# Kernel optimization log

Hardware: AMD Instinct MI355X
Metric: run time of the kernel (lower is better)

## Reference

```python
import jax, jax.numpy as jnp
import numpy as np

N, E, G = 10000, 100000, 64
NB, EMB, S, COUT, LMAX = 16, 16, 8, 16, 2
RMAX = 4.0
WNUM = (LMAX + 1) * COUT * S * S  # 3072 per-edge TP weights


def setup_inputs() -> dict:
    key = jax.random.key(0)
    ks = jax.random.split(key, 16)
    def lin(k, i, o):
        return (jax.random.normal(k, (i, o), jnp.float32) / np.sqrt(i)).astype(jnp.float32)
    return {
        "pos": jax.random.normal(ks[0], (N, 3), jnp.float32),
        "A": jax.random.randint(ks[1], (N,), 0, 10),
        "batch": jnp.sort(jax.random.randint(ks[2], (N,), 0, G)),
        "edge_src": jax.random.randint(ks[3], (E,), 0, N),
        "edge_dst": jax.random.randint(ks[4], (E,), 0, N),
        "edge_shifts": jnp.zeros((E, 3), jnp.float32),
        "cell": jax.random.normal(ks[5], (G, 3, 3), jnp.float32),
        "emb_table": jax.random.normal(ks[6], (10, EMB), jnp.float32),
        "mlp_w1": lin(ks[7], EMB, 64), "mlp_b1": jnp.zeros((64,), jnp.float32),
        "mlp_w2": lin(ks[8], 64, S), "mlp_b2": jnp.zeros((S,), jnp.float32),
        "fc_w1": lin(ks[9], NB, 64), "fc_b1": jnp.zeros((64,), jnp.float32),
        "fc_w2": lin(ks[10], 64, 64), "fc_b2": jnp.zeros((64,), jnp.float32),
        "fc_w3": lin(ks[11], 64, WNUM), "fc_b3": jnp.zeros((WNUM,), jnp.float32),
    }


def _forward(pos, edge_shifts, cell, emb_table, mlp_w1, mlp_b1, mlp_w2, mlp_b2,
             fc_w1, fc_b1, fc_w2, fc_b2, fc_w3, fc_b3, A, batch, edge_src, edge_dst):
    # periodic-image edge vectors: shifts @ cell[graph of src node]
    shift = jnp.einsum('ei,eij->ej', edge_shifts, cell[batch[edge_src]])
    vec = pos[edge_dst] - pos[edge_src] + shift                     # (E,3)
    r = jnp.linalg.norm(vec, axis=1)                                # (E,)
    n = vec / jnp.maximum(r, 1e-9)[:, None]                         # unit edge direction
    # per-node scalar features: atom_mlp(atom_embedding(A))
    Ai = jax.nn.silu(emb_table[A] @ mlp_w1 + mlp_b1) @ mlp_w2 + mlp_b2  # (N,S)
    # radial basis: gaussian soft-one-hot on [0, RMAX] with cutoff, * sqrt(NB)
    vals = jnp.linspace(0.0, RMAX, NB + 2)[1:-1]
    step = RMAX / (NB + 1)
    emb = jnp.exp(-(((r[:, None] - vals) / step) ** 2)) / 1.12 * np.sqrt(NB)  # (E,NB)
    # radial MLP -> per-edge tensor-product weights
    h = jax.nn.silu(emb @ fc_w1 + fc_b1)
    h = jax.nn.silu(h @ fc_w2 + fc_b2)
    W = (h @ fc_w3 + fc_b3).reshape(E, LMAX + 1, COUT, S, S)        # (E,L,Cout,C1,C2)
    # f_in rank-L block is Ai[src] x n^{(x)L}; x2 is scalar Ai[dst].
    # The Cartesian TP factorizes: channel mixing once, then attach n^{(x)L}.
    fs, fd = Ai[edge_src], Ai[edge_dst]                             # (E,S)
    m = jnp.einsum('eloab,ea,eb->elo', W, fs, fd)                   # (E,L,Cout)
    out0 = m[:, 0]                                                  # (E,Cout)       rank 0
    out1 = m[:, 1, :, None] * n[:, None, :]                         # (E,Cout,3)     rank 1
    n2 = n[:, :, None] * n[:, None, :]                              # (E,3,3)
    out2 = m[:, 2, :, None, None] * n2[:, None]                     # (E,Cout,3,3)   rank 2
    ef = jnp.concatenate([out0, out1.reshape(E, -1), out2.reshape(E, -1)], axis=-1)  # (E, 13*Cout)
    # scatter-sum to destination nodes, normalize by neighbor count (clamped to 1)
    cnt = jnp.maximum(jax.ops.segment_sum(jnp.ones((E,), ef.dtype), edge_dst, num_segments=N), 1.0)
    return jax.ops.segment_sum(ef, edge_dst, num_segments=N) / cnt[:, None]  # (N, 208)


def reference(pos, A, batch, edge_src, edge_dst, edge_shifts, cell, emb_table,
              mlp_w1, mlp_b1, mlp_w2, mlp_b2, fc_w1, fc_b1, fc_w2, fc_b2, fc_w3, fc_b3):
    return _forward(pos, edge_shifts, cell, emb_table, mlp_w1, mlp_b1, mlp_w2, mlp_b2,
                    fc_w1, fc_b1, fc_w2, fc_b2, fc_w3, fc_b3, A, batch, edge_src, edge_dst)
```

## Files before the change

kernel.cpp:

```cpp
#include <hip/hip_runtime.h>
#include <math.h>
#include <stdint.h>


typedef float  f32x4  __attribute__((ext_vector_type(4)));
typedef short  s16x8  __attribute__((ext_vector_type(8)));
typedef __bf16 bf16x8 __attribute__((ext_vector_type(8)));

__device__ __forceinline__ float silu_f(float x) {
    return x / (1.0f + __expf(-x));
}

__device__ __forceinline__ void split8(f32x4 a, f32x4 b, s16x8& hi, s16x8& lo) {
    bf16x8 h8, l8;
    #pragma unroll
    for (int i = 0; i < 4; ++i) {
        float z = a[i]; __bf16 zh = (__bf16)z; h8[i] = zh; l8[i] = (__bf16)(z - (float)zh);
        float y = b[i]; __bf16 yh = (__bf16)y; h8[4 + i] = yh; l8[4 + i] = (__bf16)(y - (float)yh);
    }
    hi = __builtin_bit_cast(s16x8, h8);
    lo = __builtin_bit_cast(s16x8, l8);
}

__global__ __launch_bounds__(256) void k_setup(const float* __restrict__ w3,
                                               const float* __restrict__ b3,
                                               ushort* __restrict__ wz,
                                               const int* __restrict__ A,
                                               const float* __restrict__ embt,
                                               const float* __restrict__ w1,
                                               const float* __restrict__ b1,
                                               const float* __restrict__ w2,
                                               const float* __restrict__ b2,
                                               float* __restrict__ Ai,
                                               const int* __restrict__ edst,
                                               int* __restrict__ deg,
                                               int N, int E, int aiB) {
    const int b = blockIdx.x;
    const int tid = threadIdx.x;
    if (b < 780) {
        int t = b * 256 + tid;
        int j    = t & 7;
        int l    = (t >> 3) & 63;
        int rest = t >> 9;
        int tt   = rest % 3;
        int s    = rest / 3;
        int lo   = tt * 16 + (l & 15);
        int kl   = (l >> 4) * 8 + j;
        float v;
        if (s < 128) {
            int ab = s >> 1;
            int c  = (s & 1) * 32 + kl;
            v = w3[c * 3072 + lo * 64 + ab];
        } else {
            int ab = (s - 128) * 32 + kl;
            v = b3[lo * 64 + ab];
        }
        __bf16 hi  = (__bf16)v;
        __bf16 lor = (__bf16)(v - (float)hi);
        size_t base = (size_t)(s * 3 + tt) * 2 * 512 + l * 8 + j;
        wz[base]       = __builtin_bit_cast(ushort, hi);
        wz[base + 512] = __builtin_bit_cast(ushort, lor);
    } else if (b < 780 + aiB) {
        int i = (b - 780) * 256 + tid;
        if (i >= N) return;
        float e[16];
        const float* er = embt + A[i] * 16;
        #pragma unroll
        for (int k = 0; k < 16; ++k) e[k] = er[k];
        float h1[64];
        #pragma unroll
        for (int j = 0; j < 64; ++j) {
            float a = b1[j];
            #pragma unroll
            for (int k = 0; k < 16; ++k) a = fmaf(e[k], w1[k * 64 + j], a);
            h1[j] = silu_f(a);
        }
        #pragma unroll
        for (int o = 0; o < 8; ++o) {
            float a = b2[o];
            #pragma unroll
            for (int j = 0; j < 64; ++j) a = fmaf(h1[j], w2[j * 8 + o], a);
            Ai[i * 8 + o] = a;
        }
    } else {
        int e = (b - 780 - aiB) * 256 + tid;
        if (e < E) atomicAdd(&deg[edst[e]], 1);
    }
}

__global__ __launch_bounds__(1024) void k_scan(const int* __restrict__ deg,
                                               int* __restrict__ offs,
                                               int* __restrict__ cursor, int N) {
    __shared__ int part[1024];
    const int t = threadIdx.x;
    const int chunk = (N + 1023) / 1024;
    const int beg = t * chunk;
    const int end = min(beg + chunk, N);
    int s = 0;
    for (int i = beg; i < end; ++i) s += deg[i];
    part[t] = s;
    __syncthreads();
    for (int off = 1; off < 1024; off <<= 1) {
        int v = (t >= off) ? part[t - off] : 0;
        __syncthreads();
        part[t] += v;
        __syncthreads();
    }
    int run = (t == 0) ? 0 : part[t - 1];
    for (int i = beg; i < end; ++i) {
        offs[i] = run;
        cursor[i] = run;
        run += deg[i];
    }
    if (t == 1023) offs[N] = part[1023];
}

__global__ __launch_bounds__(256, 2) void k_edge(
    const float* __restrict__ pos, const int* __restrict__ batch,
    const int* __restrict__ esrc, const int* __restrict__ edst,
    const float* __restrict__ eshift, const float* __restrict__ cell,
    const float* __restrict__ fw1, const float* __restrict__ fb1,
    const float* __restrict__ fw2, const float* __restrict__ fb2,
    const ushort* __restrict__ wz,
    const float* __restrict__ Ai, float* __restrict__ ef,
    int* __restrict__ cursor, int* __restrict__ eidx, int E) {

    __shared__ __align__(16) float s_un[8704];
    __shared__ __align__(16) float s_o[8704];

    const int tid  = threadIdx.x;
    const int lane = tid & 63;
    const int w    = __builtin_amdgcn_readfirstlane(tid >> 6);
    const int e0   = blockIdx.x * 128;
    const int j0   = w * 16;

    const f32x4* wzv = reinterpret_cast<const f32x4*>(wz);

    s16x8 Ba[12], Bb[12];
#define LOADB(ARR, U) { \
    const f32x4* gs = wzv + (size_t)(U) * 768 + lane; \
    _Pragma("unroll") \
    for (int f = 0; f < 12; ++f) ARR[f] = __builtin_bit_cast(s16x8, gs[f * 64]); }

    LOADB(Ba, 0);

    #pragma unroll
    for (int rr = 0; rr < 2; ++rr) {
        const int e = e0 + rr * 64 + lane;
        const bool valid = (e < E);
        const int ec = valid ? e : (E - 1);
        const int src = esrc[ec];
        const int dst = edst[ec];

        const int g0 = batch[src];
        const float s0 = eshift[ec * 3 + 0], s1 = eshift[ec * 3 + 1], s2 = eshift[ec * 3 + 2];
        const float* cl = cell + g0 * 9;
        float vx = pos[dst * 3 + 0] - pos[src * 3 + 0] + s0 * cl[0] + s1 * cl[3] + s2 * cl[6];
        float vy = pos[dst * 3 + 1] - pos[src * 3 + 1] + s0 * cl[1] + s1 * cl[4] + s2 * cl[7];
        float vz = pos[dst * 3 + 2] - pos[src * 3 + 2] + s0 * cl[2] + s1 * cl[5] + s2 * cl[8];
        float r = sqrtf(vx * vx + vy * vy + vz * vz);
        float rinv = 1.0f / fmaxf(r, 1e-9f);
        float nx = vx * rinv, ny = vy * rinv, nz = vz * rinv;

        float embv[16];
        const float step = 4.0f / 17.0f;
        const float sc = 4.0f / 1.12f;
        #pragma unroll
        for (int k = 0; k < 16; ++k) {
            float d = (r - (float)(k + 1) * step) / step;
            embv[k] = __expf(-d * d) * sc;
        }

        const int hb = (rr * 64 + lane) * 65;
        #pragma unroll
        for (int jj = 0; jj < 16; ++jj) {
            const int j = j0 + jj;
            float a = fb1[j];
            #pragma unroll
            for (int k = 0; k < 16; ++k) a = fmaf(embv[k], fw1[k * 64 + j], a);
            s_un[hb + j] = silu_f(a);
        }

        {
            const float* As = Ai + (size_t)src * 8;
            const float* Ad = Ai + (size_t)dst * 8;
            float fsa0 = As[2 * w], fsa1 = As[2 * w + 1];
            f32x4 d0 = *reinterpret_cast<const f32x4*>(Ad);
            f32x4 d1 = *reinterpret_cast<const f32x4*>(Ad + 4);
            float fdv[8] = {d0[0], d0[1], d0[2], d0[3], d1[0], d1[1], d1[2], d1[3]};
            const int ob = (rr * 64 + lane) * 68 + j0;
            #pragma unroll
            for (int i = 0; i < 8; ++i)  s_o[ob + i]     = fsa0 * fdv[i];
            #pragma unroll
            for (int i = 0; i < 8; ++i)  s_o[ob + 8 + i] = fsa1 * fdv[i];
        }

        if (w == 0 && valid) {
            float* np = ef + (size_t)e * 52;
            np[48] = nx; np[49] = ny; np[50] = nz;
            int pp = atomicAdd(&cursor[dst], 1);
            eidx[pp] = e;
        }
    }
    __syncthreads();

    float hcr[2][16];
    #pragma unroll
    for (int rr = 0; rr < 2; ++rr) {
        const int hb = (rr * 64 + lane) * 65;
        #pragma unroll
        for (int i = 0; i < 16; ++i) hcr[rr][i] = fb2[j0 + i];
        #pragma unroll 4
        for (int j = 0; j < 64; ++j) {
            const float v = s_un[hb + j];
            const float* w2r = fw2 + j * 64 + j0;
            #pragma unroll
            for (int i = 0; i < 16; ++i) hcr[rr][i] = fmaf(v, w2r[i], hcr[rr][i]);
        }
        #pragma unroll
        for (int i = 0; i < 16; ++i) hcr[rr][i] = silu_f(hcr[rr][i]);
    }
    __syncthreads();

    #pragma unroll
    for (int rr = 0; rr < 2; ++rr) {
        const int hb = (rr * 64 + lane) * 68 + j0;
        #pragma unroll
        for (int i = 0; i < 16; ++i) s_un[hb + i] = hcr[rr][i];
    }
    __syncthreads();

    LOADB(Bb, 64);

    const int g = lane >> 4;
    const int mrow = w * 32 + (lane & 15);
    s16x8 AhF[2][2], AlF[2][2], OhF[2][2], OlF[2][2];
    #pragma unroll
    for (int mt = 0; mt < 2; ++mt) {
        const float* hr = s_un + (mrow + mt * 16) * 68;
        const float* orw = s_o + (mrow + mt * 16) * 68;
        f32x4 a0 = *reinterpret_cast<const f32x4*>(hr + g * 8);
        f32x4 a1 = *reinterpret_cast<const f32x4*>(hr + g * 8 + 4);
        split8(a0, a1, AhF[mt][0], AlF[mt][0]);
        f32x4 a2 = *reinterpret_cast<const f32x4*>(hr + 32 + g * 8);
        f32x4 a3 = *reinterpret_cast<const f32x4*>(hr + 32 + g * 8 + 4);
        split8(a2, a3, AhF[mt][1], AlF[mt][1]);
        f32x4 o0 = *reinterpret_cast<const f32x4*>(orw + g * 8);
        f32x4 o1 = *reinterpret_cast<const f32x4*>(orw + g * 8 + 4);
        split8(o0, o1, OhF[mt][0], OlF[mt][0]);
        f32x4 o2 = *reinterpret_cast<const f32x4*>(orw + 32 + g * 8);
        f32x4 o3 = *reinterpret_cast<const f32x4*>(orw + 32 + g * 8 + 4);
        split8(o2, o3, OhF[mt][1], OlF[mt][1]);
    }

    const int rb = w * 32 + (lane >> 4) * 4;

    f32x4 acc[2][3];
    #pragma unroll
    for (int mt = 0; mt < 2; ++mt)
        #pragma unroll
        for (int t = 0; t < 3; ++t) acc[mt][t] = (f32x4){0.f, 0.f, 0.f, 0.f};

    __builtin_amdgcn_s_setprio(1);
    #pragma unroll
    for (int t = 0; t < 3; ++t) {
        #pragma unroll
        for (int sl = 0; sl < 2; ++sl) {
            s16x8 Bh = Bb[(sl * 3 + t) * 2];
            s16x8 Bl = Bb[(sl * 3 + t) * 2 + 1];
            acc[0][t] = __builtin_amdgcn_mfma_f32_16x16x32_bf16(OhF[0][sl], Bh, acc[0][t], 0, 0, 0);
            acc[0][t] = __builtin_amdgcn_mfma_f32_16x16x32_bf16(OhF[0][sl], Bl, acc[0][t], 0, 0, 0);
            acc[0][t] = __builtin_amdgcn_mfma_f32_16x16x32_bf16(OlF[0][sl], Bh, acc[0][t], 0, 0, 0);
            acc[1][t] = __builtin_amdgcn_mfma_f32_16x16x32_bf16(OhF[1][sl], Bh, acc[1][t], 0, 0, 0);
            acc[1][t] = __builtin_amdgcn_mfma_f32_16x16x32_bf16(OhF[1][sl], Bl, acc[1][t], 0, 0, 0);
            acc[1][t] = __builtin_amdgcn_mfma_f32_16x16x32_bf16(OlF[1][sl], Bh, acc[1][t], 0, 0, 0);
        }
    }
    __builtin_amdgcn_s_setprio(0);

#define MSTEP(BC, U) { \
    float ov[8]; \
    _Pragma("unroll") \
    for (int i = 0; i < 4; ++i) { \
        ov[i]     = s_o[(rb + i) * 68 + (U)]; \
        ov[4 + i] = s_o[(rb + 16 + i) * 68 + (U)]; \
    } \
    __builtin_amdgcn_s_setprio(1); \
    _Pragma("unroll") \
    for (int t = 0; t < 3; ++t) { \
        f32x4 D0 = {0.f, 0.f, 0.f, 0.f}; \
        f32x4 D1 = {0.f, 0.f, 0.f, 0.f}; \
        _Pragma("unroll") \
        for (int sl = 0; sl < 2; ++sl) { \
            s16x8 Bh = BC[(sl * 3 + t) * 2]; \
            s16x8 Bl = BC[(sl * 3 + t) * 2 + 1]; \
            D0 = __builtin_amdgcn_mfma_f32_16x16x32_bf16(AhF[0][sl], Bh, D0, 0, 0, 0); \
            D0 = __builtin_amdgcn_mfma_f32_16x16x32_bf16(AhF[0][sl], Bl, D0, 0, 0, 0); \
            D0 = __builtin_amdgcn_mfma_f32_16x16x32_bf16(AlF[0][sl], Bh, D0, 0, 0, 0); \
            D1 = __builtin_amdgcn_mfma_f32_16x16x32_bf16(AhF[1][sl], Bh, D1, 0, 0, 0); \
            D1 = __builtin_amdgcn_mfma_f32_16x16x32_bf16(AhF[1][sl], Bl, D1, 0, 0, 0); \
            D1 = __builtin_amdgcn_mfma_f32_16x16x32_bf16(AlF[1][sl], Bh, D1, 0, 0, 0); \
        } \
        __builtin_amdgcn_s_setprio(0); \
        _Pragma("unroll") \
        for (int i = 0; i < 4; ++i) { \
            acc[0][t][i] = fmaf(ov[i],     D0[i], acc[0][t][i]); \
            acc[1][t][i] = fmaf(ov[4 + i], D1[i], acc[1][t][i]); \
        } \
        __builtin_amdgcn_s_setprio(1); \
    } \
    __builtin_amdgcn_s_setprio(0); }

    for (int u = 0; u < 64; u += 2) {
        LOADB(Bb, u + 1);
        MSTEP(Ba, u);
        if (u + 2 < 64) LOADB(Ba, u + 2);
        MSTEP(Bb, u + 1);
    }
#undef MSTEP
#undef LOADB

    #pragma unroll
    for (int mt = 0; mt < 2; ++mt) {
        #pragma unroll
        for (int t = 0; t < 3; ++t) {
            #pragma unroll
            for (int i = 0; i < 4; ++i) {
                const int ee = e0 + rb + mt * 16 + i;
                if (ee < E) ef[(size_t)ee * 52 + t * 16 + (lane & 15)] = acc[mt][t][i];
            }
        }
    }
}

__global__ __launch_bounds__(256) void k_gather(const float* __restrict__ ef,
                                                const int* __restrict__ offs,
                                                const int* __restrict__ eidx,
                                                float* __restrict__ out, int N) {
    const int lane = threadIdx.x & 63;
    const int node = blockIdx.x * 4 + (threadIdx.x >> 6);
    if (node >= N) return;

    const int beg = offs[node];
    const int end = offs[node + 1];

    int mi[4], ii[4], jj[4], mode[4];
    #pragma unroll
    for (int t = 0; t < 4; ++t) {
        int c = lane + 64 * t;
        if (c < 16)       { mi[t] = c;                 ii[t] = 0;     jj[t] = 0;     mode[t] = 0; }
        else if (c < 64)  { int u = c - 16; mi[t] = 16 + u / 3; ii[t] = u % 3; jj[t] = 0; mode[t] = 1; }
        else if (c < 208) { int u = c - 64; mi[t] = 32 + u / 9; int rr = u % 9; ii[t] = rr / 3; jj[t] = rr % 3; mode[t] = 2; }
        else              { mi[t] = 0; ii[t] = 0; jj[t] = 0; mode[t] = 3; }
    }

    float acc[4] = {0.f, 0.f, 0.f, 0.f};
    for (int k = beg; k < end; ++k) {
        const int e = eidx[k];
        const float* b = ef + (size_t)e * 52;
        float v = (lane < 51) ? b[lane] : 0.0f;
        float n0 = __shfl(v, 48);
        float n1 = __shfl(v, 49);
        float n2 = __shfl(v, 50);
        #pragma unroll
        for (int t = 0; t < 4; ++t) {
            float mval = __shfl(v, mi[t]);
            float ni = (ii[t] == 0) ? n0 : ((ii[t] == 1) ? n1 : n2);
            float nj = (jj[t] == 0) ? n0 : ((jj[t] == 1) ? n1 : n2);
            float f  = (mode[t] == 0) ? 1.0f
                     : (mode[t] == 1) ? ni
                     : (mode[t] == 2) ? ni * nj
                     : 0.0f;
            acc[t] = fmaf(mval, f, acc[t]);
        }
    }

    const float inv = 1.0f / fmaxf((float)(end - beg), 1.0f);
    float* op = out + (size_t)node * 208;
    op[lane]        = acc[0] * inv;
    op[lane + 64]   = acc[1] * inv;
    op[lane + 128]  = acc[2] * inv;
    if (lane < 16) op[lane + 192] = acc[3] * inv;
}

extern "C" void kernel_launch(void* const* d_in, const int* in_sizes, int n_in,
                              void* d_out, int out_size, void* d_ws, size_t ws_size,
                              hipStream_t stream) {
    const float* pos    = (const float*)d_in[0];
    const int*   A      = (const int*)d_in[1];
    const int*   batch  = (const int*)d_in[2];
    const int*   esrc   = (const int*)d_in[3];
    const int*   edst   = (const int*)d_in[4];
    const float* eshift = (const float*)d_in[5];
    const float* cell   = (const float*)d_in[6];
    const float* embt   = (const float*)d_in[7];
    const float* mw1    = (const float*)d_in[8];
    const float* mb1    = (const float*)d_in[9];
    const float* mw2    = (const float*)d_in[10];
    const float* mb2    = (const float*)d_in[11];
    const float* fw1    = (const float*)d_in[12];
    const float* fb1    = (const float*)d_in[13];
    const float* fw2    = (const float*)d_in[14];
    const float* fb2    = (const float*)d_in[15];
    const float* w3     = (const float*)d_in[16];
    const float* b3     = (const float*)d_in[17];
    float* out = (float*)d_out;

    const int N = in_sizes[1];
    const int E = in_sizes[3];

    char* p = (char*)d_ws;
    auto take = [&](size_t bytes) {
        char* q = p;
        p += (bytes + 255) & ~(size_t)255;
        return q;
    };
    ushort* wz    = (ushort*)take((size_t)130 * 3 * 2 * 512 * sizeof(ushort));
    float* Ai     = (float*)take((size_t)N * 8 * sizeof(float));
    int*   deg    = (int*)  take((size_t)N * sizeof(int));
    int*   offs   = (int*)  take((size_t)(N + 1) * sizeof(int));
    int*   cursor = (int*)  take((size_t)N * sizeof(int));
    int*   eidx   = (int*)  take((size_t)E * sizeof(int));
    float* ef     = (float*)take((size_t)E * 52 * sizeof(float));

    hipMemsetAsync(deg, 0, (size_t)N * sizeof(int), stream);

    const int aiB = (N + 255) / 256;
    const int histB = (E + 255) / 256;
    k_setup<<<780 + aiB + histB, 256, 0, stream>>>(w3, b3, wz, A, embt, mw1, mb1,
                                                   mw2, mb2, Ai, edst, deg, N, E, aiB);
    k_scan<<<1, 1024, 0, stream>>>(deg, offs, cursor, N);
    k_edge<<<(E + 127) / 128, 256, 0, stream>>>(pos, batch, esrc, edst, eshift, cell,
                                                fw1, fb1, fw2, fb2, wz, Ai,
                                                ef, cursor, eidx, E);
    k_gather<<<(N + 3) / 4, 256, 0, stream>>>(ef, offs, eidx, out, N);
}
```

Measured before the change: 244.4 us.

## Halve edge-kernel block to two waves, each handling 64 edges with 4 M-tiles

The edge kernel moves from 4 waves of 32 edges each to 2 waves of 64 edges each, launched as 128-thread blocks. Each B fragment loaded from the weight table now feeds four MFMA row tiles instead of two, which halves global weight traffic per edge. The radial MLP is computed in two passes through a smaller shared staging buffer, and each wave takes its A fragments in its own pass. In exchange, register pressure roughly doubles for accumulators and fragments, occupancy falls, and more barriers are added.

Measured after the change: 310.8 us. +27.2%, slower.

```diff
diff --git a/kernel.cpp b/kernel.cpp
--- a/kernel.cpp
+++ b/kernel.cpp
@@ -115,7 +115,7 @@
     if (t == 1023) offs[N] = part[1023];
 }
 
-__global__ __launch_bounds__(256, 2) void k_edge(
+__global__ __launch_bounds__(128, 1) void k_edge(
     const float* __restrict__ pos, const int* __restrict__ batch,
     const int* __restrict__ esrc, const int* __restrict__ edst,
     const float* __restrict__ eshift, const float* __restrict__ cell,
@@ -125,26 +125,25 @@
     const float* __restrict__ Ai, float* __restrict__ ef,
     int* __restrict__ cursor, int* __restrict__ eidx, int E) {
 
-    __shared__ __align__(16) float s_un[8704];
-    __shared__ __align__(16) float s_o[8704];
+    __shared__ __align__(16) float s_st[64 * 68];
+    __shared__ __align__(16) float s_o[128 * 68];
 
     const int tid  = threadIdx.x;
     const int lane = tid & 63;
     const int w    = __builtin_amdgcn_readfirstlane(tid >> 6);
     const int e0   = blockIdx.x * 128;
-    const int j0   = w * 16;
+    const int j0   = w * 32;
+    const int g    = lane >> 4;
 
     const f32x4* wzv = reinterpret_cast<const f32x4*>(wz);
-
     s16x8 Ba[12], Bb[12];
+    s16x8 AhF[4][2], AlF[4][2];
+
 #define LOADB(ARR, U) { \
     const f32x4* gs = wzv + (size_t)(U) * 768 + lane; \
     _Pragma("unroll") \
     for (int f = 0; f < 12; ++f) ARR[f] = __builtin_bit_cast(s16x8, gs[f * 64]); }
 
-    LOADB(Ba, 0);
-
-    #pragma unroll
     for (int rr = 0; rr < 2; ++rr) {
         const int e = e0 + rr * 64 + lane;
         const bool valid = (e < E);
@@ -171,28 +170,25 @@
             embv[k] = __expf(-d * d) * sc;
         }
 
-        const int hb = (rr * 64 + lane) * 65;
-        #pragma unroll
-        for (int jj = 0; jj < 16; ++jj) {
+        #pragma unroll
+        for (int jj = 0; jj < 32; ++jj) {
             const int j = j0 + jj;
             float a = fb1[j];
             #pragma unroll
             for (int k = 0; k < 16; ++k) a = fmaf(embv[k], fw1[k * 64 + j], a);
-            s_un[hb + j] = silu_f(a);
+            s_st[lane * 65 + j] = silu_f(a);
         }
 
         {
             const float* As = Ai + (size_t)src * 8;
             const float* Ad = Ai + (size_t)dst * 8;
-            float fsa0 = As[2 * w], fsa1 = As[2 * w + 1];
+            f32x4 fsa = *reinterpret_cast<const f32x4*>(As + 4 * w);
             f32x4 d0 = *reinterpret_cast<const f32x4*>(Ad);
             f32x4 d1 = *reinterpret_cast<const f32x4*>(Ad + 4);
             float fdv[8] = {d0[0], d0[1], d0[2], d0[3], d1[0], d1[1], d1[2], d1[3]};
             const int ob = (rr * 64 + lane) * 68 + j0;
             #pragma unroll
-            for (int i = 0; i < 8; ++i)  s_o[ob + i]     = fsa0 * fdv[i];
-            #pragma unroll
-            for (int i = 0; i < 8; ++i)  s_o[ob + 8 + i] = fsa1 * fdv[i];
+            for (int i = 0; i < 32; ++i) s_o[ob + i] = fsa[i >> 3] * fdv[i & 7];
         }
 
         if (w == 0 && valid) {
@@ -201,50 +197,46 @@
             int pp = atomicAdd(&cursor[dst], 1);
             eidx[pp] = e;
         }
-    }
-    __syncthreads();
-
-    float hcr[2][16];
-    #pragma unroll
-    for (int rr = 0; rr < 2; ++rr) {
-        const int hb = (rr * 64 + lane) * 65;
-        #pragma unroll
-        for (int i = 0; i < 16; ++i) hcr[rr][i] = fb2[j0 + i];
+        __syncthreads();
+
+        float hcr[32];
+        #pragma unroll
+        for (int i = 0; i < 32; ++i) hcr[i] = fb2[j0 + i];
         #pragma unroll 4
         for (int j = 0; j < 64; ++j) {
-            const float v = s_un[hb + j];
+            const float v = s_st[lane * 65 + j];
             const float* w2r = fw2 + j * 64 + j0;
             #pragma unroll
-            for (int i = 0; i < 16; ++i) hcr[rr][i] = fmaf(v, w2r[i], hcr[rr][i]);
-        }
-        #pragma unroll
-        for (int i = 0; i < 16; ++i) hcr[rr][i] = silu_f(hcr[rr][i]);
-    }
-    __syncthreads();
-
-    #pragma unroll
-    for (int rr = 0; rr < 2; ++rr) {
-        const int hb = (rr * 64 + lane) * 68 + j0;
-        #pragma unroll
-        for (int i = 0; i < 16; ++i) s_un[hb + i] = hcr[rr][i];
-    }
-    __syncthreads();
+            for (int i = 0; i < 32; ++i) hcr[i] = fmaf(v, w2r[i], hcr[i]);
+        }
+        #pragma unroll
+        for (int i = 0; i < 32; ++i) hcr[i] = silu_f(hcr[i]);
+        __syncthreads();
+
+        #pragma unroll
+        for (int i = 0; i < 32; ++i) s_st[lane * 68 + j0 + i] = hcr[i];
+        __syncthreads();
+
+        if (w == rr) {
+            #pragma unroll
+            for (int mt = 0; mt < 4; ++mt) {
+                const float* hr = s_st + ((lane & 15) + mt * 16) * 68;
+                f32x4 a0 = *reinterpret_cast<const f32x4*>(hr + g * 8);
+                f32x4 a1 = *reinterpret_cast<const f32x4*>(hr + g * 8 + 4);
+                split8(a0, a1, AhF[mt][0], AlF[mt][0]);
+                f32x4 a2 = *reinterpret_cast<const f32x4*>(hr + 32 + g * 8);
+                f32x4 a3 = *reinterpret_cast<const f32x4*>(hr + 32 + g * 8 + 4);
+                split8(a2, a3, AhF[mt][1], AlF[mt][1]);
+            }
+        }
+        __syncthreads();
+    }
 
     LOADB(Bb, 64);
-
-    const int g = lane >> 4;
-    const int mrow = w * 32 + (lane & 15);
-    s16x8 AhF[2][2], AlF[2][2], OhF[2][2], OlF[2][2];
-    #pragma unroll
-    for (int mt = 0; mt < 2; ++mt) {
-        const float* hr = s_un + (mrow + mt * 16) * 68;
-        const float* orw = s_o + (mrow + mt * 16) * 68;
-        f32x4 a0 = *reinterpret_cast<const f32x4*>(hr + g * 8);
-        f32x4 a1 = *reinterpret_cast<const f32x4*>(hr + g * 8 + 4);
-        split8(a0, a1, AhF[mt][0], AlF[mt][0]);
-        f32x4 a2 = *reinterpret_cast<const f32x4*>(hr + 32 + g * 8);
-        f32x4 a3 = *reinterpret_cast<const f32x4*>(hr + 32 + g * 8 + 4);
-        split8(a2, a3, AhF[mt][1], AlF[mt][1]);
+    s16x8 OhF[4][2], OlF[4][2];
+    #pragma unroll
+    for (int mt = 0; mt < 4; ++mt) {
+        const float* orw = s_o + (w * 64 + mt * 16 + (lane & 15)) * 68;
         f32x4 o0 = *reinterpret_cast<const f32x4*>(orw + g * 8);
         f32x4 o1 = *reinterpret_cast<const f32x4*>(orw + g * 8 + 4);
         split8(o0, o1, OhF[mt][0], OlF[mt][0]);
@@ -253,11 +245,9 @@
         split8(o2, o3, OhF[mt][1], OlF[mt][1]);
     }
 
-    const int rb = w * 32 + (lane >> 4) * 4;
-
-    f32x4 acc[2][3];
-    #pragma unroll
-    for (int mt = 0; mt < 2; ++mt)
+    f32x4 acc[4][3];
+    #pragma unroll
+    for (int mt = 0; mt < 4; ++mt)
         #pragma unroll
         for (int t = 0; t < 3; ++t) acc[mt][t] = (f32x4){0.f, 0.f, 0.f, 0.f};
 
@@ -268,28 +258,34 @@
         for (int sl = 0; sl < 2; ++sl) {
             s16x8 Bh = Bb[(sl * 3 + t) * 2];
             s16x8 Bl = Bb[(sl * 3 + t) * 2 + 1];
-            acc[0][t] = __builtin_amdgcn_mfma_f32_16x16x32_bf16(OhF[0][sl], Bh, acc[0][t], 0, 0, 0);
-            acc[0][t] = __builtin_amdgcn_mfma_f32_16x16x32_bf16(OhF[0][sl], Bl, acc[0][t], 0, 0, 0);
-            acc[0][t] = __builtin_amdgcn_mfma_f32_16x16x32_bf16(OlF[0][sl], Bh, acc[0][t], 0, 0, 0);
-            acc[1][t] = __builtin_amdgcn_mfma_f32_16x16x32_bf16(OhF[1][sl], Bh, acc[1][t], 0, 0, 0);
-            acc[1][t] = __builtin_amdgcn_mfma_f32_16x16x32_bf16(OhF[1][sl], Bl, acc[1][t], 0, 0, 0);
-            acc[1][t] = __builtin_amdgcn_mfma_f32_16x16x32_bf16(OlF[1][sl], Bh, acc[1][t], 0, 0, 0);
+            #pragma unroll
+            for (int mt = 0; mt < 4; ++mt) {
+                acc[mt][t] = __builtin_amdgcn_mfma_f32_16x16x32_bf16(OhF[mt][sl], Bh, acc[mt][t], 0, 0, 0);
+                acc[mt][t] = __builtin_amdgcn_mfma_f32_16x16x32_bf16(OhF[mt][sl], Bl, acc[mt][t], 0, 0, 0);
+                acc[mt][t] = __builtin_amdgcn_mfma_f32_16x16x32_bf16(OlF[mt][sl], Bh, acc[mt][t], 0, 0, 0);
+            }
         }
     }
     __builtin_amdgcn_s_setprio(0);
 
+    LOADB(Ba, 0);
+
+    const int rbase = w * 64 + (lane >> 4) * 4;
+
 #define MSTEP(BC, U) { \
-    float ov[8]; \
+    float ov[16]; \
     _Pragma("unroll") \
-    for (int i = 0; i < 4; ++i) { \
-        ov[i]     = s_o[(rb + i) * 68 + (U)]; \
-        ov[4 + i] = s_o[(rb + 16 + i) * 68 + (U)]; \
-    } \
+    for (int mt = 0; mt < 4; ++mt) \
+        _Pragma("unroll") \
+        for (int i = 0; i < 4; ++i) \
+            ov[mt * 4 + i] = s_o[(rbase + mt * 16 + i) * 68 + (U)]; \
     __builtin_amdgcn_s_setprio(1); \
     _Pragma("unroll") \
     for (int t = 0; t < 3; ++t) { \
         f32x4 D0 = {0.f, 0.f, 0.f, 0.f}; \
         f32x4 D1 = {0.f, 0.f, 0.f, 0.f}; \
+        f32x4 D2 = {0.f, 0.f, 0.f, 0.f}; \
+        f32x4 D3 = {0.f, 0.f, 0.f, 0.f}; \
         _Pragma("unroll") \
         for (int sl = 0; sl < 2; ++sl) { \
             s16x8 Bh = BC[(sl * 3 + t) * 2]; \
@@ -300,12 +296,20 @@
             D1 = __builtin_amdgcn_mfma_f32_16x16x32_bf16(AhF[1][sl], Bh, D1, 0, 0, 0); \
             D1 = __builtin_amdgcn_mfma_f32_16x16x32_bf16(AhF[1][sl], Bl, D1, 0, 0, 0); \
             D1 = __builtin_amdgcn_mfma_f32_16x16x32_bf16(AlF[1][sl], Bh, D1, 0, 0, 0); \
+            D2 = __builtin_amdgcn_mfma_f32_16x16x32_bf16(AhF[2][sl], Bh, D2, 0, 0, 0); \
+            D2 = __builtin_amdgcn_mfma_f32_16x16x32_bf16(AhF[2][sl], Bl, D2, 0, 0, 0); \
+            D2 = __builtin_amdgcn_mfma_f32_16x16x32_bf16(AlF[2][sl], Bh, D2, 0, 0, 0); \
+            D3 = __builtin_amdgcn_mfma_f32_16x16x32_bf16(AhF[3][sl], Bh, D3, 0, 0, 0); \
+            D3 = __builtin_amdgcn_mfma_f32_16x16x32_bf16(AhF[3][sl], Bl, D3, 0, 0, 0); \
+            D3 = __builtin_amdgcn_mfma_f32_16x16x32_bf16(AlF[3][sl], Bh, D3, 0, 0, 0); \
         } \
         __builtin_amdgcn_s_setprio(0); \
         _Pragma("unroll") \
         for (int i = 0; i < 4; ++i) { \
-            acc[0][t][i] = fmaf(ov[i],     D0[i], acc[0][t][i]); \
-            acc[1][t][i] = fmaf(ov[4 + i], D1[i], acc[1][t][i]); \
+            acc[0][t][i] = fmaf(ov[i],      D0[i], acc[0][t][i]); \
+            acc[1][t][i] = fmaf(ov[4 + i],  D1[i], acc[1][t][i]); \
+            acc[2][t][i] = fmaf(ov[8 + i],  D2[i], acc[2][t][i]); \
+            acc[3][t][i] = fmaf(ov[12 + i], D3[i], acc[3][t][i]); \
         } \
         __builtin_amdgcn_s_setprio(1); \
     } \
@@ -321,12 +325,12 @@
 #undef LOADB
 
     #pragma unroll
-    for (int mt = 0; mt < 2; ++mt) {
+    for (int mt = 0; mt < 4; ++mt) {
         #pragma unroll
         for (int t = 0; t < 3; ++t) {
             #pragma unroll
             for (int i = 0; i < 4; ++i) {
-                const int ee = e0 + rb + mt * 16 + i;
+                const int ee = e0 + rbase + mt * 16 + i;
                 if (ee < E) ef[(size_t)ee * 52 + t * 16 + (lane & 15)] = acc[mt][t][i];
             }
         }
@@ -430,7 +434,7 @@
     k_setup<<<780 + aiB + histB, 256, 0, stream>>>(w3, b3, wz, A, embt, mw1, mb1,
                                                    mw2, mb2, Ai, edst, deg, N, E, aiB);
     k_scan<<<1, 1024, 0, stream>>>(deg, offs, cursor, N);
-    k_edge<<<(E + 127) / 128, 256, 0, stream>>>(pos, batch, esrc, edst, eshift, cell,
+    k_edge<<<(E + 127) / 128, 128, 0, stream>>>(pos, batch, esrc, edst, eshift, cell,
                                                 fw1, fb1, fw2, fb2, wz, Ai,
                                                 ef, cursor, eidx, E);
     k_gather<<<(N + 3) / 4, 256, 0, stream>>>(ef, offs, eidx, out, N);
```

## Process edge halves sequentially through a half-size LDS staging buffer

Applied to the files above, without the earlier changes.

The edge kernel's hidden-layer staging buffer is halved and the two 64-edge halves are processed one after another, not both at once. Each half's layer-2 result is staged and immediately split into bf16 hi/lo A fragments by the two waves that own those rows. This cuts LDS use and live registers (one hcr array, not two), which should allow higher occupancy, at the cost of extra block barriers and a loop that is no longer unrolled. The gather kernel's per-node edge loop also gets an unroll-4 hint.

Measured after the change: 262.5 us. 1.07x slower.

```diff
diff --git a/kernel.cpp b/kernel.cpp
--- a/kernel.cpp
+++ b/kernel.cpp
@@ -125,7 +125,7 @@
     const float* __restrict__ Ai, float* __restrict__ ef,
     int* __restrict__ cursor, int* __restrict__ eidx, int E) {
 
-    __shared__ __align__(16) float s_un[8704];
+    __shared__ __align__(16) float s_st[4352];
     __shared__ __align__(16) float s_o[8704];
 
     const int tid  = threadIdx.x;
@@ -144,7 +144,9 @@
 
     LOADB(Ba, 0);
 
-    #pragma unroll
+    const int g = lane >> 4;
+    s16x8 AhF[2][2], AlF[2][2];
+
     for (int rr = 0; rr < 2; ++rr) {
         const int e = e0 + rr * 64 + lane;
         const bool valid = (e < E);
@@ -171,14 +173,13 @@
             embv[k] = __expf(-d * d) * sc;
         }
 
-        const int hb = (rr * 64 + lane) * 65;
         #pragma unroll
         for (int jj = 0; jj < 16; ++jj) {
             const int j = j0 + jj;
             float a = fb1[j];
             #pragma unroll
             for (int k = 0; k < 16; ++k) a = fmaf(embv[k], fw1[k * 64 + j], a);
-            s_un[hb + j] = silu_f(a);
+            s_st[lane * 65 + j] = silu_f(a);
         }
 
         {
@@ -201,50 +202,49 @@
             int pp = atomicAdd(&cursor[dst], 1);
             eidx[pp] = e;
         }
-    }
-    __syncthreads();
-
-    float hcr[2][16];
-    #pragma unroll
-    for (int rr = 0; rr < 2; ++rr) {
-        const int hb = (rr * 64 + lane) * 65;
-        #pragma unroll
-        for (int i = 0; i < 16; ++i) hcr[rr][i] = fb2[j0 + i];
+        __syncthreads();
+
+        float hcr[16];
+        #pragma unroll
+        for (int i = 0; i < 16; ++i) hcr[i] = fb2[j0 + i];
         #pragma unroll 4
         for (int j = 0; j < 64; ++j) {
-            const float v = s_un[hb + j];
+            const float v = s_st[lane * 65 + j];
             const float* w2r = fw2 + j * 64 + j0;
             #pragma unroll
-            for (int i = 0; i < 16; ++i) hcr[rr][i] = fmaf(v, w2r[i], hcr[rr][i]);
-        }
-        #pragma unroll
-        for (int i = 0; i < 16; ++i) hcr[rr][i] = silu_f(hcr[rr][i]);
-    }
-    __syncthreads();
-
-    #pragma unroll
-    for (int rr = 0; rr < 2; ++rr) {
-        const int hb = (rr * 64 + lane) * 68 + j0;
-        #pragma unroll
-        for (int i = 0; i < 16; ++i) s_un[hb + i] = hcr[rr][i];
-    }
-    __syncthreads();
+            for (int i = 0; i < 16; ++i) hcr[i] = fmaf(v, w2r[i], hcr[i]);
+        }
+        #pragma unroll
+        for (int i = 0; i < 16; ++i) hcr[i] = silu_f(hcr[i]);
+        __syncthreads();
+
+        #pragma unroll
+        for (int i = 0; i < 16; ++i) s_st[lane * 68 + j0 + i] = hcr[i];
+        __syncthreads();
+
+        if ((w >> 1) == rr) {
+            const int lrow = (w & 1) * 32 + (lane & 15);
+            #pragma unroll
+            for (int mt = 0; mt < 2; ++mt) {
+                const float* hr = s_st + (lrow + mt * 16) * 68;
+                f32x4 a0 = *reinterpret_cast<const f32x4*>(hr + g * 8);
+                f32x4 a1 = *reinterpret_cast<const f32x4*>(hr + g * 8 + 4);
+                split8(a0, a1, AhF[mt][0], AlF[mt][0]);
+                f32x4 a2 = *reinterpret_cast<const f32x4*>(hr + 32 + g * 8);
+                f32x4 a3 = *reinterpret_cast<const f32x4*>(hr + 32 + g * 8 + 4);
+                split8(a2, a3, AhF[mt][1], AlF[mt][1]);
+            }
+        }
+        __syncthreads();
+    }
 
     LOADB(Bb, 64);
 
-    const int g = lane >> 4;
     const int mrow = w * 32 + (lane & 15);
-    s16x8 AhF[2][2], AlF[2][2], OhF[2][2], OlF[2][2];
+    s16x8 OhF[2][2], OlF[2][2];
     #pragma unroll
     for (int mt = 0; mt < 2; ++mt) {
-        const float* hr = s_un + (mrow + mt * 16) * 68;
         const float* orw = s_o + (mrow + mt * 16) * 68;
-        f32x4 a0 = *reinterpret_cast<const f32x4*>(hr + g * 8);
-        f32x4 a1 = *reinterpret_cast<const f32x4*>(hr + g * 8 + 4);
-        split8(a0, a1, AhF[mt][0], AlF[mt][0]);
-        f32x4 a2 = *reinterpret_cast<const f32x4*>(hr + 32 + g * 8);
-        f32x4 a3 = *reinterpret_cast<const f32x4*>(hr + 32 + g * 8 + 4);
-        split8(a2, a3, AhF[mt][1], AlF[mt][1]);
         f32x4 o0 = *reinterpret_cast<const f32x4*>(orw + g * 8);
         f32x4 o1 = *reinterpret_cast<const f32x4*>(orw + g * 8 + 4);
         split8(o0, o1, OhF[mt][0], OlF[mt][0]);
@@ -355,6 +355,7 @@
     }
 
     float acc[4] = {0.f, 0.f, 0.f, 0.f};
+    #pragma unroll 4
     for (int k = beg; k < end; ++k) {
         const int e = eidx[k];
         const float* b = ef + (size_t)e * 52;
```
